# Kernel tuning notes

Measured on AMD Instinct MI355X. Metric: run time of the kernel, lower is better.

Reference implementation:

```python
import jax, jax.numpy as jnp
import numpy as np

N = 100000   # nodes
E = 1600000  # edges
F = 13       # input features
H = 128      # hidden dim
G = 512      # graphs in batch
C = 10       # classes
EPS = 1e-5   # BatchNorm eps


def setup_inputs() -> dict:
    key = jax.random.key(0)
    ks = jax.random.split(key, 12)
    inp = {
        "x": jax.random.normal(ks[0], (N, F), dtype=jnp.float32),
        "edge_index": jax.random.randint(ks[1], (2, E), 0, N, dtype=jnp.int64),
        "batch": jnp.sort(jax.random.randint(ks[2], (N,), 0, G, dtype=jnp.int64)),
        "W1": jax.random.normal(ks[3], (F, H), dtype=jnp.float32) / np.sqrt(F),
        "b1": jnp.zeros((H,), jnp.float32),
        "g1": jnp.ones((H,), jnp.float32), "be1": jnp.zeros((H,), jnp.float32),
        "m1": jnp.zeros((H,), jnp.float32), "v1": jnp.ones((H,), jnp.float32),
        "W2": jax.random.normal(ks[4], (H, H), dtype=jnp.float32) / np.sqrt(H),
        "b2": jnp.zeros((H,), jnp.float32),
        "g2": jnp.ones((H,), jnp.float32), "be2": jnp.zeros((H,), jnp.float32),
        "m2": jnp.zeros((H,), jnp.float32), "v2": jnp.ones((H,), jnp.float32),
        "W3": jax.random.normal(ks[5], (H, H), dtype=jnp.float32) / np.sqrt(H),
        "b3": jnp.zeros((H,), jnp.float32),
        "g3": jnp.ones((H,), jnp.float32), "be3": jnp.zeros((H,), jnp.float32),
        "m3": jnp.zeros((H,), jnp.float32), "v3": jnp.ones((H,), jnp.float32),
        "Wc1": jax.random.normal(ks[6], (H, H // 2), dtype=jnp.float32) / np.sqrt(H),
        "bc1": jnp.zeros((H // 2,), jnp.float32),
        "Wc2": jax.random.normal(ks[7], (H // 2, C), dtype=jnp.float32) / np.sqrt(H // 2),
        "bc2": jnp.zeros((C,), jnp.float32),
    }
    return inp


def reference(x, edge_index, batch,
              W1, b1, g1, be1, m1, v1,
              W2, b2, g2, be2, m2, v2,
              W3, b3, g3, be3, m3, v3,
              Wc1, bc1, Wc2, bc2):
    src, dst = edge_index[0], edge_index[1]
    n = x.shape[0]
    # GCN symmetric norm with self-loops: deg = in-degree(A) + 1
    deg = jax.ops.segment_sum(jnp.ones(src.shape[0], x.dtype), dst, num_segments=n) + 1.0
    dis = jax.lax.rsqrt(deg)                    # D^{-1/2}
    enorm = dis[src] * dis[dst]                 # per-edge norm [E]
    snorm = dis * dis                           # self-loop norm [N]

    def gcn(h, W, b):
        h = h @ W                               # [N,H]
        msg = h[src] * enorm[:, None]           # gather + scale [E,H]
        agg = jax.ops.segment_sum(msg, dst, num_segments=n)  # scatter-add
        return agg + h * snorm[:, None] + b

    def bn(h, g, be, m, v):                     # eval-mode BatchNorm1d
        return (h - m) * jax.lax.rsqrt(v + EPS) * g + be

    h = jax.nn.relu(bn(gcn(x, W1, b1), g1, be1, m1, v1))
    h = jax.nn.relu(bn(gcn(h, W2, b2), g2, be2, m2, v2))
    h = jax.nn.relu(bn(gcn(h, W3, b3), g3, be3, m3, v3))
    # dropout is identity in eval mode

    # global mean pool over graphs
    sums = jax.ops.segment_sum(h, batch, num_segments=G)            # [G,H]
    cnts = jax.ops.segment_sum(jnp.ones(n, h.dtype), batch, num_segments=G)
    pooled = sums / jnp.maximum(cnts, 1.0)[:, None]

    hid = jax.nn.relu(pooled @ Wc1 + bc1)
    logits = hid @ Wc2 + bc2                                        # [G,C]
    return logits
```

## Files before the change

kernel.cpp:

```cpp
#include <hip/hip_runtime.h>
#include <hip/hip_bf16.h>

#define EPS 1e-5f

typedef unsigned short u16;
typedef unsigned int u32;
typedef __attribute__((ext_vector_type(8))) short bf16x8;
typedef __attribute__((ext_vector_type(4))) float f32x4;

__device__ __forceinline__ u32 f2bf(float f) {
  u32 u = __float_as_uint(f);
  return (u + 0x7FFFu + ((u >> 16) & 1u)) >> 16;
}
__device__ __forceinline__ u32 pack2bf(float lo, float hi) {
  return f2bf(lo) | (f2bf(hi) << 16);
}

__device__ __forceinline__ void dacc(float2& a, u32 u) {
  a.x += __uint_as_float(u << 16);
  a.y += __uint_as_float(u & 0xFFFF0000u);
}

__global__ void k_hist_rank(const int* __restrict__ dst, int* __restrict__ cnt,
                            int* __restrict__ rank, int E) {
  int i = blockIdx.x * blockDim.x + threadIdx.x;
  int i8 = i << 3;
  if (i8 + 7 < E) {
    int4 da = *(const int4*)(dst + i8);
    int4 db = *(const int4*)(dst + i8 + 4);
    int r0 = atomicAdd(&cnt[da.x], 1);
    int r1 = atomicAdd(&cnt[da.y], 1);
    int r2 = atomicAdd(&cnt[da.z], 1);
    int r3 = atomicAdd(&cnt[da.w], 1);
    int r4 = atomicAdd(&cnt[db.x], 1);
    int r5 = atomicAdd(&cnt[db.y], 1);
    int r6 = atomicAdd(&cnt[db.z], 1);
    int r7 = atomicAdd(&cnt[db.w], 1);
    *(int4*)(rank + i8)     = make_int4(r0, r1, r2, r3);
    *(int4*)(rank + i8 + 4) = make_int4(r4, r5, r6, r7);
  } else {
    for (int e = i8; e < E; ++e) rank[e] = atomicAdd(&cnt[dst[e]], 1);
  }
}

__global__ void k_prep_nodes(const int* __restrict__ cnt, const float* __restrict__ x,
                             float* __restrict__ dis, int* __restrict__ pdeg,
                             float* __restrict__ xs, int N) {
  int n = blockIdx.x * blockDim.x + threadIdx.x;
  if (n > N) return;
  if (n == N) {
#pragma unroll
    for (int f = 0; f < 16; f += 4)
      *(float4*)(xs + (size_t)N * 16 + f) = make_float4(0.f, 0.f, 0.f, 0.f);
    return;
  }
  int d = cnt[n];
  float dn = rsqrtf((float)d + 1.0f);
  dis[n] = dn;
  pdeg[n] = (d + 3) & ~3;
  float v[16];
#pragma unroll
  for (int f = 0; f < 13; ++f) v[f] = x[(size_t)n * 13 + f] * dn;
  v[13] = v[14] = v[15] = 0.f;
#pragma unroll
  for (int f = 0; f < 16; f += 4)
    *(float4*)(xs + (size_t)n * 16 + f) = make_float4(v[f], v[f+1], v[f+2], v[f+3]);
}

__global__ void k_scan_block(const int* __restrict__ in, int* __restrict__ out,
                             int* __restrict__ bsum, int N) {
  __shared__ int tmp[256];
  int lid = threadIdx.x;
  int i = blockIdx.x * 256 + lid;
  int v = (i < N) ? in[i] : 0;
  tmp[lid] = v;
  __syncthreads();
  for (int off = 1; off < 256; off <<= 1) {
    int t = (lid >= off) ? tmp[lid - off] : 0;
    __syncthreads();
    tmp[lid] += t;
    __syncthreads();
  }
  if (i < N) out[i] = tmp[lid] - v;
  if (lid == 255) bsum[blockIdx.x] = tmp[255];
}

__global__ void k_scan_bsum(const int* __restrict__ bsum, int* __restrict__ bexc, int nb) {
  __shared__ int tmp[512];
  int lid = threadIdx.x;
  int v = (lid < nb) ? bsum[lid] : 0;
  tmp[lid] = v;
  __syncthreads();
  for (int off = 1; off < 512; off <<= 1) {
    int t = (lid >= off) ? tmp[lid - off] : 0;
    __syncthreads();
    tmp[lid] += t;
    __syncthreads();
  }
  if (lid < nb) bexc[lid] = tmp[lid] - v;
}

__global__ void k_add_back_pad(int* __restrict__ offs, const int* __restrict__ bexc,
                               const int* __restrict__ bsum, const int* __restrict__ deg,
                               const int* __restrict__ pdeg, int* __restrict__ csr,
                               int N, int nb) {
  int i = blockIdx.x * 256 + threadIdx.x;
  if (i < N) {
    int o = offs[i] + bexc[blockIdx.x];
    offs[i] = o;
    int b = o + deg[i], e = o + pdeg[i];
    for (int j = b; j < e; ++j) csr[j] = N;
  }
  if (i == 0) offs[N] = bexc[nb - 1] + bsum[nb - 1];
}

__global__ void k_fill_rank(const int* __restrict__ src, const int* __restrict__ dst,
                            const int* __restrict__ rank, const int* __restrict__ offs,
                            int* __restrict__ csr, int E) {
  int i = blockIdx.x * blockDim.x + threadIdx.x;
  int i4 = i << 2;
  if (i4 + 3 < E) {
    int s0 = src[i4], s1 = src[i4 + 1], s2 = src[i4 + 2], s3 = src[i4 + 3];
    int d0 = dst[i4], d1 = dst[i4 + 1], d2 = dst[i4 + 2], d3 = dst[i4 + 3];
    int r0 = rank[i4], r1 = rank[i4 + 1], r2 = rank[i4 + 2], r3 = rank[i4 + 3];
    csr[offs[d0] + r0] = s0;
    csr[offs[d1] + r1] = s1;
    csr[offs[d2] + r2] = s2;
    csr[offs[d3] + r3] = s3;
  } else {
    for (int e = i4; e < E; ++e) csr[offs[dst[e]] + rank[e]] = src[e];
  }
}

__global__ void k_prep_w(const float* __restrict__ W2, const float* __restrict__ W3,
                         const float* __restrict__ b2, const float* __restrict__ g2,
                         const float* __restrict__ be2, const float* __restrict__ m2,
                         const float* __restrict__ v2,
                         const float* __restrict__ b3, const float* __restrict__ g3,
                         const float* __restrict__ be3, const float* __restrict__ m3,
                         const float* __restrict__ v3,
                         u16* __restrict__ Wht2, u16* __restrict__ Wlt2,
                         u16* __restrict__ Wht3, u16* __restrict__ Wlt3,
                         float* __restrict__ sc2, float* __restrict__ tc2,
                         float* __restrict__ sc3, float* __restrict__ tc3) {
  int idx = blockIdx.x * 256 + threadIdx.x;
  int layer = idx >> 14;
  int e = idx & 16383;
  int c = e >> 7, k = e & 127;
  const float* W = layer ? W3 : W2;
  float w = W[k * 128 + c];
  u32 h = f2bf(w);
  float l = w - __uint_as_float(h << 16);
  u16* Wh = layer ? Wht3 : Wht2;
  u16* Wl = layer ? Wlt3 : Wlt2;
  Wh[e] = (u16)h;
  Wl[e] = (u16)f2bf(l);
  if (e < 128) {
    int ch = e;
    const float* gg = layer ? g3 : g2;  const float* vv = layer ? v3 : v2;
    const float* be = layer ? be3 : be2; const float* mm = layer ? m3 : m2;
    const float* bb = layer ? b3 : b2;
    float s = gg[ch] * rsqrtf(vv[ch] + EPS);
    (layer ? sc3 : sc2)[ch] = s;
    (layer ? tc3 : tc2)[ch] = be[ch] + (bb[ch] - mm[ch]) * s;
  }
}

__global__ __launch_bounds__(64) void k_agg16(
    const float* __restrict__ xs, const int* __restrict__ csr,
    const int* __restrict__ offs, const float* __restrict__ dis,
    float* __restrict__ out, int N) {
  int node = (blockIdx.x << 2) + (threadIdx.x >> 4);
  if (node >= N) return;
  int f = threadIdx.x & 15;
  float a0 = xs[(size_t)node * 16 + f];
  float a1 = 0.f, a2 = 0.f, a3 = 0.f;
  int beg = offs[node], end = offs[node + 1];
  for (int i = beg; i < end; i += 4) {
    int4 s4 = *(const int4*)(csr + i);
    a0 += xs[(size_t)s4.x * 16 + f];
    a1 += xs[(size_t)s4.y * 16 + f];
    a2 += xs[(size_t)s4.z * 16 + f];
    a3 += xs[(size_t)s4.w * 16 + f];
  }
  out[(size_t)node * 16 + f] = dis[node] * ((a0 + a1) + (a2 + a3));
}

__global__ __launch_bounds__(256) void k_gemm1(
    const float* __restrict__ ax, const float* __restrict__ W1,
    const float* __restrict__ bb, const float* __restrict__ gg,
    const float* __restrict__ be, const float* __restrict__ mm,
    const float* __restrict__ vv, const float* __restrict__ dis,
    u32* __restrict__ outb, int N) {
  const int lane = threadIdx.x & 63;
  const int wid = blockIdx.x * (blockDim.x >> 6) + (threadIdx.x >> 6);
  const int nw = gridDim.x * (blockDim.x >> 6);
  const int c0 = lane * 2, c1 = c0 + 1;
  float s0 = gg[c0] * rsqrtf(vv[c0] + EPS);
  float t0 = be[c0] + (bb[c0] - mm[c0]) * s0;
  float s1 = gg[c1] * rsqrtf(vv[c1] + EPS);
  float t1 = be[c1] + (bb[c1] - mm[c1]) * s1;
  float w0[13], w1[13];
#pragma unroll
  for (int k = 0; k < 13; ++k) {
    w0[k] = W1[k * 128 + c0];
    w1[k] = W1[k * 128 + c1];
  }
  for (int node = wid; node <= N; node += nw) {
    if (node == N) { outb[(size_t)node * 64 + lane] = 0u; continue; }
    float4 A0 = *(const float4*)(ax + (size_t)node * 16);
    float4 A1 = *(const float4*)(ax + (size_t)node * 16 + 4);
    float4 A2 = *(const float4*)(ax + (size_t)node * 16 + 8);
    float  a12 = ax[(size_t)node * 16 + 12];
    float av[13] = {A0.x, A0.y, A0.z, A0.w, A1.x, A1.y, A1.z, A1.w,
                    A2.x, A2.y, A2.z, A2.w, a12};
    float acc0 = 0.f, acc1 = 0.f;
#pragma unroll
    for (int k = 0; k < 13; ++k) {
      acc0 = fmaf(av[k], w0[k], acc0);
      acc1 = fmaf(av[k], w1[k], acc1);
    }
    float dn = dis[node];
    float o0 = dn * fmaxf(fmaf(acc0, s0, t0), 0.f);
    float o1 = dn * fmaxf(fmaf(acc1, s1, t1), 0.f);
    outb[(size_t)node * 64 + lane] = pack2bf(o0, o1);
  }
}

__global__ __launch_bounds__(256) void k_agg128(
    const u16* __restrict__ hb, const int* __restrict__ csr,
    const int* __restrict__ offs, const float* __restrict__ dis,
    uint4* __restrict__ Ahp, uint4* __restrict__ Alp, int N) {
  int node = (blockIdx.x << 2) + (threadIdx.x >> 6);
  if (node >= N) return;
  node = __builtin_amdgcn_readfirstlane(node);
  const int lane = threadIdx.x & 63;
  const int qt = lane >> 4;
  const int q = lane & 15;
  const uint4* __restrict__ H = (const uint4*)hb;
  int beg = offs[node], end = offs[node + 1];

  float2 z2 = make_float2(0.f, 0.f);
  float2 aA0 = z2, aA1 = z2, aA2 = z2, aA3 = z2;
  float2 aB0 = z2, aB1 = z2, aB2 = z2, aB3 = z2;

  {
    uint4 su = H[(size_t)node * 16 + q];
    if (qt == 0) { dacc(aA0, su.x); dacc(aA1, su.y); dacc(aA2, su.z); dacc(aA3, su.w); }
  }

  int i = beg;
  for (; i + 8 <= end; i += 8) {
    int4 sA = *(const int4*)(csr + i);
    int4 sB = *(const int4*)(csr + i + 4);
    int ea = (qt == 0) ? sA.x : (qt == 1) ? sA.y : (qt == 2) ? sA.z : sA.w;
    int eb = (qt == 0) ? sB.x : (qt == 1) ? sB.y : (qt == 2) ? sB.z : sB.w;
    uint4 uA = H[(size_t)ea * 16 + q];
    uint4 uB = H[(size_t)eb * 16 + q];
    dacc(aA0, uA.x); dacc(aA1, uA.y); dacc(aA2, uA.z); dacc(aA3, uA.w);
    dacc(aB0, uB.x); dacc(aB1, uB.y); dacc(aB2, uB.z); dacc(aB3, uB.w);
  }
  if (i < end) {
    int4 sA = *(const int4*)(csr + i);
    int ea = (qt == 0) ? sA.x : (qt == 1) ? sA.y : (qt == 2) ? sA.z : sA.w;
    uint4 uA = H[(size_t)ea * 16 + q];
    dacc(aA0, uA.x); dacc(aA1, uA.y); dacc(aA2, uA.z); dacc(aA3, uA.w);
  }

  float r[8];
  r[0] = aA0.x + aB0.x; r[1] = aA0.y + aB0.y;
  r[2] = aA1.x + aB1.x; r[3] = aA1.y + aB1.y;
  r[4] = aA2.x + aB2.x; r[5] = aA2.y + aB2.y;
  r[6] = aA3.x + aB3.x; r[7] = aA3.y + aB3.y;
#pragma unroll
  for (int j = 0; j < 8; ++j) {
    r[j] += __shfl_xor(r[j], 16, 64);
    r[j] += __shfl_xor(r[j], 32, 64);
  }
  if (qt == 0) {
    float dn = dis[node];
    uint4 ph, pl;
    u32 hw[8];
#pragma unroll
    for (int j = 0; j < 8; ++j) { r[j] *= dn; hw[j] = f2bf(r[j]); }
    ph.x = hw[0] | (hw[1] << 16);
    ph.y = hw[2] | (hw[3] << 16);
    ph.z = hw[4] | (hw[5] << 16);
    ph.w = hw[6] | (hw[7] << 16);
    float l[8];
#pragma unroll
    for (int j = 0; j < 8; ++j) l[j] = r[j] - __uint_as_float(hw[j] << 16);
    pl.x = pack2bf(l[0], l[1]);
    pl.y = pack2bf(l[2], l[3]);
    pl.z = pack2bf(l[4], l[5]);
    pl.w = pack2bf(l[6], l[7]);
    Ahp[(size_t)node * 16 + q] = ph;
    Alp[(size_t)node * 16 + q] = pl;
  }
}

template <int MODE>
__global__ __launch_bounds__(256) void k_gemm_mfma(
    const u16* __restrict__ Ah, const u16* __restrict__ Al,
    const u16* __restrict__ Wht, const u16* __restrict__ Wlt,
    const float* __restrict__ sc, const float* __restrict__ tc,
    const float* __restrict__ dis,
    u16* __restrict__ outb, int N) {
  const int lane = threadIdx.x & 63;
  const int wv = threadIdx.x >> 6;
  const int r0 = blockIdx.x * 128 + wv * 32;
  const int lr = lane & 15;
  const int kg = lane >> 4;

  bf16x8 ahf[2][4], alf[2][4];
#pragma unroll
  for (int rt = 0; rt < 2; ++rt) {
    int row = min(r0 + rt * 16 + lr, N - 1);
    const bf16x8* pAh = (const bf16x8*)(Ah + (size_t)row * 128 + kg * 8);
    const bf16x8* pAl = (const bf16x8*)(Al + (size_t)row * 128 + kg * 8);
#pragma unroll
    for (int ks = 0; ks < 4; ++ks) {
      ahf[rt][ks] = pAh[ks * 4];
      alf[rt][ks] = pAl[ks * 4];
    }
  }
  float dr[2][4];
  if (MODE == 0) {
#pragma unroll
    for (int rt = 0; rt < 2; ++rt)
#pragma unroll
      for (int j = 0; j < 4; ++j)
        dr[rt][j] = dis[min(r0 + rt * 16 + kg * 4 + j, N - 1)];
  }

#pragma unroll
  for (int ct = 0; ct < 8; ++ct) {
    int c = ct * 16 + lr;
    const bf16x8* pBh = (const bf16x8*)(Wht + (size_t)c * 128 + kg * 8);
    const bf16x8* pBl = (const bf16x8*)(Wlt + (size_t)c * 128 + kg * 8);
    bf16x8 bh[4], bl[4];
#pragma unroll
    for (int ks = 0; ks < 4; ++ks) { bh[ks] = pBh[ks * 4]; bl[ks] = pBl[ks * 4]; }
    float s = sc[c], t = tc[c];
#pragma unroll
    for (int rt = 0; rt < 2; ++rt) {
      f32x4 acc = {0.f, 0.f, 0.f, 0.f};
#pragma unroll
      for (int ks = 0; ks < 4; ++ks) {
        acc = __builtin_amdgcn_mfma_f32_16x16x32_bf16(ahf[rt][ks], bh[ks], acc, 0, 0, 0);
        acc = __builtin_amdgcn_mfma_f32_16x16x32_bf16(alf[rt][ks], bh[ks], acc, 0, 0, 0);
        acc = __builtin_amdgcn_mfma_f32_16x16x32_bf16(ahf[rt][ks], bl[ks], acc, 0, 0, 0);
      }
#pragma unroll
      for (int j = 0; j < 4; ++j) {
        int row = r0 + rt * 16 + kg * 4 + j;
        if (row < N) {
          float o = fmaxf(fmaf(acc[j], s, t), 0.f);
          if (MODE == 0) o *= dr[rt][j];
          outb[(size_t)row * 128 + c] = (u16)f2bf(o);
        }
      }
    }
  }
}

__global__ __launch_bounds__(128) void k_pool(
    const u16* __restrict__ hb, const int* __restrict__ batch,
    float* __restrict__ pooled, int N) {
  int f = threadIdx.x;
  int n0 = blockIdx.x * 128;
  int nEnd = min(n0 + 128, N);
  float acc = 0.f;
  int cur = -1;
  for (int nn = n0; nn < nEnd; ++nn) {
    int g = batch[nn];
    if (g != cur) {
      if (cur >= 0) atomicAdd(&pooled[cur * 128 + f], acc);
      cur = g;
      acc = 0.f;
    }
    acc += __uint_as_float((u32)hb[(size_t)nn * 128 + f] << 16);
  }
  if (cur >= 0) atomicAdd(&pooled[cur * 128 + f], acc);
}

__global__ __launch_bounds__(64) void k_cls(
    const float* __restrict__ pooled, const int* __restrict__ batch, int N,
    const float* __restrict__ Wc1, const float* __restrict__ bc1,
    const float* __restrict__ Wc2, const float* __restrict__ bc2,
    float* __restrict__ out, int G) {
  __shared__ float pm[128];
  __shared__ float hid[64];
  __shared__ float invc_s;
  int g = blockIdx.x, t = threadIdx.x;
  if (t == 0) {
    int lo = 0, hi = N;
    while (lo < hi) { int m = (lo + hi) >> 1; if (batch[m] < g) lo = m + 1; else hi = m; }
    int lb = lo;
    lo = 0; hi = N;
    while (lo < hi) { int m = (lo + hi) >> 1; if (batch[m] <= g) lo = m + 1; else hi = m; }
    invc_s = 1.f / fmaxf((float)(lo - lb), 1.f);
  }
  __syncthreads();
  float invc = invc_s;
  pm[t]      = pooled[g * 128 + t] * invc;
  pm[t + 64] = pooled[g * 128 + 64 + t] * invc;
  __syncthreads();
  float a = bc1[t];
#pragma unroll 8
  for (int k = 0; k < 128; ++k) a = fmaf(pm[k], Wc1[k * 64 + t], a);
  hid[t] = fmaxf(a, 0.f);
  __syncthreads();
  if (t < 10) {
    float a2 = bc2[t];
#pragma unroll
    for (int j = 0; j < 64; ++j) a2 = fmaf(hid[j], Wc2[j * 10 + t], a2);
    out[g * 10 + t] = a2;
  }
}

extern "C" void kernel_launch(void* const* d_in, const int* in_sizes, int n_in,
                              void* d_out, int out_size, void* d_ws, size_t ws_size,
                              hipStream_t stream) {
  const float* x   = (const float*)d_in[0];
  const int*   ei  = (const int*)d_in[1];
  const int* batch = (const int*)d_in[2];
  const float* W1 = (const float*)d_in[3];
  const float* b1 = (const float*)d_in[4];
  const float* g1 = (const float*)d_in[5];
  const float* be1 = (const float*)d_in[6];
  const float* m1 = (const float*)d_in[7];
  const float* v1 = (const float*)d_in[8];
  const float* W2 = (const float*)d_in[9];
  const float* b2 = (const float*)d_in[10];
  const float* g2 = (const float*)d_in[11];
  const float* be2 = (const float*)d_in[12];
  const float* m2 = (const float*)d_in[13];
  const float* v2 = (const float*)d_in[14];
  const float* W3 = (const float*)d_in[15];
  const float* b3 = (const float*)d_in[16];
  const float* g3 = (const float*)d_in[17];
  const float* be3 = (const float*)d_in[18];
  const float* m3 = (const float*)d_in[19];
  const float* v3 = (const float*)d_in[20];
  const float* Wc1 = (const float*)d_in[21];
  const float* bc1 = (const float*)d_in[22];
  const float* Wc2 = (const float*)d_in[23];
  const float* bc2 = (const float*)d_in[24];

  const int N = in_sizes[0] / 13;
  const int E = in_sizes[1] / 2;
  const int G = out_size / 10;
  const int* src = ei;
  const int* dst = ei + E;

  char* ws = (char*)d_ws;
  size_t off = 0;
  auto alloc = [&](size_t bytes) {
    char* p = ws + off;
    off = (off + bytes + 255) & ~(size_t)255;
    return p;
  };
  int*   deg    = (int*)  alloc((size_t)N * 4);
  float* dis    = (float*)alloc((size_t)N * 4);
  int*   pdeg   = (int*)  alloc((size_t)N * 4);
  int*   offs   = (int*)  alloc((size_t)(N + 1) * 4);
  const int nb  = (N + 255) / 256;
  int*   bsum   = (int*)  alloc((size_t)nb * 4);
  int*   bexc   = (int*)  alloc((size_t)nb * 4);
  int*   rank   = (int*)  alloc((size_t)E * 4);
  int*   csr    = (int*)  alloc(((size_t)E + 3 * (size_t)N + 8) * 4);
  u16*   hbf    = (u16*)  alloc((size_t)(N + 1) * 128 * 2);
  u16*   Ahp    = (u16*)  alloc((size_t)N * 128 * 2);
  u16*   Alp    = (u16*)  alloc((size_t)N * 128 * 2);
  float* xs     = (float*)alloc((size_t)(N + 1) * 16 * 4);
  u16*   Wht2   = (u16*)  alloc(16384 * 2);
  u16*   Wlt2   = (u16*)  alloc(16384 * 2);
  u16*   Wht3   = (u16*)  alloc(16384 * 2);
  u16*   Wlt3   = (u16*)  alloc(16384 * 2);
  float* sc2    = (float*)alloc(128 * 4);
  float* tc2    = (float*)alloc(128 * 4);
  float* sc3    = (float*)alloc(128 * 4);
  float* tc3    = (float*)alloc(128 * 4);
  float* pooled = (float*)alloc((size_t)G * 128 * 4);
  float* ax = (float*)Ahp;

  hipMemsetAsync(deg, 0, (size_t)N * 4, stream);
  hipMemsetAsync(pooled, 0, (size_t)G * 128 * 4, stream);

  k_prep_w<<<128, 256, 0, stream>>>(W2, W3, b2, g2, be2, m2, v2, b3, g3, be3, m3, v3,
                                    Wht2, Wlt2, Wht3, Wlt3, sc2, tc2, sc3, tc3);

  const int nE8 = (E + 7) / 8;
  k_hist_rank<<<(nE8 + 255) / 256, 256, 0, stream>>>(dst, deg, rank, E);
  k_prep_nodes<<<(N + 256) / 256, 256, 0, stream>>>(deg, x, dis, pdeg, xs, N);
  k_scan_block<<<nb, 256, 0, stream>>>(pdeg, offs, bsum, N);
  k_scan_bsum<<<1, 512, 0, stream>>>(bsum, bexc, nb);
  k_add_back_pad<<<nb, 256, 0, stream>>>(offs, bexc, bsum, deg, pdeg, csr, N, nb);
  const int nE4 = (E + 3) / 4;
  k_fill_rank<<<(nE4 + 255) / 256, 256, 0, stream>>>(src, dst, rank, offs, csr, E);

  k_agg16<<<(N + 3) / 4, 64, 0, stream>>>(xs, csr, offs, dis, ax, N);
  k_gemm1<<<1024, 256, 0, stream>>>(ax, W1, b1, g1, be1, m1, v1, dis, (u32*)hbf, N);

  const int gemmGrid = (N + 127) / 128;
  k_agg128<<<(N + 3) / 4, 256, 0, stream>>>(hbf, csr, offs, dis,
                                            (uint4*)Ahp, (uint4*)Alp, N);
  k_gemm_mfma<0><<<gemmGrid, 256, 0, stream>>>(Ahp, Alp, Wht2, Wlt2, sc2, tc2, dis,
                                               hbf, N);
  k_agg128<<<(N + 3) / 4, 256, 0, stream>>>(hbf, csr, offs, dis,
                                            (uint4*)Ahp, (uint4*)Alp, N);
  k_gemm_mfma<1><<<gemmGrid, 256, 0, stream>>>(Ahp, Alp, Wht3, Wlt3, sc3, tc3, dis,
                                               hbf, N);

  k_pool<<<(N + 127) / 128, 128, 0, stream>>>(hbf, batch, pooled, N);
  k_cls<<<G, 64, 0, stream>>>(pooled, batch, N, Wc1, bc1, Wc2, bc2, (float*)d_out, G);
}
```

Measured before the change: 532.6 us.

## Fuse neighbor aggregation with MFMA GEMM via LDS staging for layers two and three

Merges the per-node 128-wide gather-aggregate kernel and the split-bf16 MFMA GEMM into one kernel. Each block aggregates 64 nodes into swizzled shared memory, then runs the GEMM straight from LDS, so the hi/lo aggregate arrays no longer round-trip through global memory. This needs ping-pong output buffers (hbf/hbf2). The two memsets are folded into the weight-prep kernel, which also zeroes the padding row. Each wave now handles 16 nodes in sequence, which cuts latency-hiding parallelism in the gather phase and leaves the MFMA phase waiting on the slowest wave in the block.

```diff
diff --git a/kernel.cpp b/kernel.cpp
--- a/kernel.cpp
+++ b/kernel.cpp
@@ -142,7 +142,9 @@
                          u16* __restrict__ Wht2, u16* __restrict__ Wlt2,
                          u16* __restrict__ Wht3, u16* __restrict__ Wlt3,
                          float* __restrict__ sc2, float* __restrict__ tc2,
-                         float* __restrict__ sc3, float* __restrict__ tc3) {
+                         float* __restrict__ sc3, float* __restrict__ tc3,
+                         int* __restrict__ deg, float* __restrict__ pooled,
+                         u32* __restrict__ hbf2_padrow, int N, int GP) {
   int idx = blockIdx.x * 256 + threadIdx.x;
   int layer = idx >> 14;
   int e = idx & 16383;
@@ -164,6 +166,9 @@
     (layer ? sc3 : sc2)[ch] = s;
     (layer ? tc3 : tc2)[ch] = be[ch] + (bb[ch] - mm[ch]) * s;
   }
+  for (int i = idx; i < N; i += 32768) deg[i] = 0;
+  for (int i = idx; i < GP; i += 32768) pooled[i] = 0.f;
+  if (idx < 64) hbf2_padrow[idx] = 0u;
 }
 
 __global__ __launch_bounds__(64) void k_agg16(
@@ -227,112 +232,103 @@
   }
 }
 
-__global__ __launch_bounds__(256) void k_agg128(
+template <int MODE>
+__global__ __launch_bounds__(256) void k_agg_gemm(
     const u16* __restrict__ hb, const int* __restrict__ csr,
     const int* __restrict__ offs, const float* __restrict__ dis,
-    uint4* __restrict__ Ahp, uint4* __restrict__ Alp, int N) {
-  int node = (blockIdx.x << 2) + (threadIdx.x >> 6);
-  if (node >= N) return;
-  node = __builtin_amdgcn_readfirstlane(node);
+    const u16* __restrict__ Wht, const u16* __restrict__ Wlt,
+    const float* __restrict__ sc, const float* __restrict__ tc,
+    u16* __restrict__ outb, int N) {
+  __shared__ uint4 Ash[64][16];
+  __shared__ uint4 Asl[64][16];
+  const int wv = threadIdx.x >> 6;
   const int lane = threadIdx.x & 63;
   const int qt = lane >> 4;
   const int q = lane & 15;
+  const int base = blockIdx.x * 64;
   const uint4* __restrict__ H = (const uint4*)hb;
-  int beg = offs[node], end = offs[node + 1];
-
-  float2 z2 = make_float2(0.f, 0.f);
-  float2 aA0 = z2, aA1 = z2, aA2 = z2, aA3 = z2;
-  float2 aB0 = z2, aB1 = z2, aB2 = z2, aB3 = z2;
-
-  {
-    uint4 su = H[(size_t)node * 16 + q];
-    if (qt == 0) { dacc(aA0, su.x); dacc(aA1, su.y); dacc(aA2, su.z); dacc(aA3, su.w); }
-  }
-
-  int i = beg;
-  for (; i + 8 <= end; i += 8) {
-    int4 sA = *(const int4*)(csr + i);
-    int4 sB = *(const int4*)(csr + i + 4);
-    int ea = (qt == 0) ? sA.x : (qt == 1) ? sA.y : (qt == 2) ? sA.z : sA.w;
-    int eb = (qt == 0) ? sB.x : (qt == 1) ? sB.y : (qt == 2) ? sB.z : sB.w;
-    uint4 uA = H[(size_t)ea * 16 + q];
-    uint4 uB = H[(size_t)eb * 16 + q];
-    dacc(aA0, uA.x); dacc(aA1, uA.y); dacc(aA2, uA.z); dacc(aA3, uA.w);
-    dacc(aB0, uB.x); dacc(aB1, uB.y); dacc(aB2, uB.z); dacc(aB3, uB.w);
-  }
-  if (i < end) {
-    int4 sA = *(const int4*)(csr + i);
-    int ea = (qt == 0) ? sA.x : (qt == 1) ? sA.y : (qt == 2) ? sA.z : sA.w;
-    uint4 uA = H[(size_t)ea * 16 + q];
-    dacc(aA0, uA.x); dacc(aA1, uA.y); dacc(aA2, uA.z); dacc(aA3, uA.w);
-  }
-
-  float r[8];
-  r[0] = aA0.x + aB0.x; r[1] = aA0.y + aB0.y;
-  r[2] = aA1.x + aB1.x; r[3] = aA1.y + aB1.y;
-  r[4] = aA2.x + aB2.x; r[5] = aA2.y + aB2.y;
-  r[6] = aA3.x + aB3.x; r[7] = aA3.y + aB3.y;
-#pragma unroll
-  for (int j = 0; j < 8; ++j) {
-    r[j] += __shfl_xor(r[j], 16, 64);
-    r[j] += __shfl_xor(r[j], 32, 64);
-  }
-  if (qt == 0) {
-    float dn = dis[node];
-    uint4 ph, pl;
-    u32 hw[8];
-#pragma unroll
-    for (int j = 0; j < 8; ++j) { r[j] *= dn; hw[j] = f2bf(r[j]); }
-    ph.x = hw[0] | (hw[1] << 16);
-    ph.y = hw[2] | (hw[3] << 16);
-    ph.z = hw[4] | (hw[5] << 16);
-    ph.w = hw[6] | (hw[7] << 16);
-    float l[8];
-#pragma unroll
-    for (int j = 0; j < 8; ++j) l[j] = r[j] - __uint_as_float(hw[j] << 16);
-    pl.x = pack2bf(l[0], l[1]);
-    pl.y = pack2bf(l[2], l[3]);
-    pl.z = pack2bf(l[4], l[5]);
-    pl.w = pack2bf(l[6], l[7]);
-    Ahp[(size_t)node * 16 + q] = ph;
-    Alp[(size_t)node * 16 + q] = pl;
-  }
-}
-
-template <int MODE>
-__global__ __launch_bounds__(256) void k_gemm_mfma(
-    const u16* __restrict__ Ah, const u16* __restrict__ Al,
-    const u16* __restrict__ Wht, const u16* __restrict__ Wlt,
-    const float* __restrict__ sc, const float* __restrict__ tc,
-    const float* __restrict__ dis,
-    u16* __restrict__ outb, int N) {
-  const int lane = threadIdx.x & 63;
-  const int wv = threadIdx.x >> 6;
-  const int r0 = blockIdx.x * 128 + wv * 32;
+
+  for (int t = 0; t < 16; ++t) {
+    int row = wv * 16 + t;
+    int node = base + row;
+    if (node >= N) break;
+    int beg = offs[node], end = offs[node + 1];
+
+    float2 z2 = make_float2(0.f, 0.f);
+    float2 aA0 = z2, aA1 = z2, aA2 = z2, aA3 = z2;
+    float2 aB0 = z2, aB1 = z2, aB2 = z2, aB3 = z2;
+    {
+      uint4 su = H[(size_t)node * 16 + q];
+      if (qt == 0) { dacc(aA0, su.x); dacc(aA1, su.y); dacc(aA2, su.z); dacc(aA3, su.w); }
+    }
+    int i = beg;
+    for (; i + 8 <= end; i += 8) {
+      int4 sA = *(const int4*)(csr + i);
+      int4 sB = *(const int4*)(csr + i + 4);
+      int ea = (qt == 0) ? sA.x : (qt == 1) ? sA.y : (qt == 2) ? sA.z : sA.w;
+      int eb = (qt == 0) ? sB.x : (qt == 1) ? sB.y : (qt == 2) ? sB.z : sB.w;
+      uint4 uA = H[(size_t)ea * 16 + q];
+      uint4 uB = H[(size_t)eb * 16 + q];
+      dacc(aA0, uA.x); dacc(aA1, uA.y); dacc(aA2, uA.z); dacc(aA3, uA.w);
+      dacc(aB0, uB.x); dacc(aB1, uB.y); dacc(aB2, uB.z); dacc(aB3, uB.w);
+    }
+    if (i < end) {
+      int4 sA = *(const int4*)(csr + i);
+      int ea = (qt == 0) ? sA.x : (qt == 1) ? sA.y : (qt == 2) ? sA.z : sA.w;
+      uint4 uA = H[(size_t)ea * 16 + q];
+      dacc(aA0, uA.x); dacc(aA1, uA.y); dacc(aA2, uA.z); dacc(aA3, uA.w);
+    }
+    float r[8];
+    r[0] = aA0.x + aB0.x; r[1] = aA0.y + aB0.y;
+    r[2] = aA1.x + aB1.x; r[3] = aA1.y + aB1.y;
+    r[4] = aA2.x + aB2.x; r[5] = aA2.y + aB2.y;
+    r[6] = aA3.x + aB3.x; r[7] = aA3.y + aB3.y;
+#pragma unroll
+    for (int j = 0; j < 8; ++j) {
+      r[j] += __shfl_xor(r[j], 16, 64);
+      r[j] += __shfl_xor(r[j], 32, 64);
+    }
+    if (qt == 0) {
+      float dn = dis[node];
+      u32 hw[8];
+      uint4 ph, pl;
+#pragma unroll
+      for (int j = 0; j < 8; ++j) { r[j] *= dn; hw[j] = f2bf(r[j]); }
+      ph.x = hw[0] | (hw[1] << 16);
+      ph.y = hw[2] | (hw[3] << 16);
+      ph.z = hw[4] | (hw[5] << 16);
+      ph.w = hw[6] | (hw[7] << 16);
+      float l[8];
+#pragma unroll
+      for (int j = 0; j < 8; ++j) l[j] = r[j] - __uint_as_float(hw[j] << 16);
+      pl.x = pack2bf(l[0], l[1]);
+      pl.y = pack2bf(l[2], l[3]);
+      pl.z = pack2bf(l[4], l[5]);
+      pl.w = pack2bf(l[6], l[7]);
+      int sw = q ^ (row & 15);
+      Ash[row][sw] = ph;
+      Asl[row][sw] = pl;
+    }
+  }
+  __syncthreads();
+
   const int lr = lane & 15;
   const int kg = lane >> 4;
-
-  bf16x8 ahf[2][4], alf[2][4];
-#pragma unroll
-  for (int rt = 0; rt < 2; ++rt) {
-    int row = min(r0 + rt * 16 + lr, N - 1);
-    const bf16x8* pAh = (const bf16x8*)(Ah + (size_t)row * 128 + kg * 8);
-    const bf16x8* pAl = (const bf16x8*)(Al + (size_t)row * 128 + kg * 8);
-#pragma unroll
-    for (int ks = 0; ks < 4; ++ks) {
-      ahf[rt][ks] = pAh[ks * 4];
-      alf[rt][ks] = pAl[ks * 4];
-    }
-  }
-  float dr[2][4];
+  const int rowbase = wv * 16;
+  const int arow = rowbase + lr;
+  bf16x8 ah[4], al[4];
+#pragma unroll
+  for (int ks = 0; ks < 4; ++ks) {
+    int b = (kg + 4 * ks) ^ (arow & 15);
+    ah[ks] = *(const bf16x8*)&Ash[arow][b];
+    al[ks] = *(const bf16x8*)&Asl[arow][b];
+  }
+  float dr[4];
   if (MODE == 0) {
 #pragma unroll
-    for (int rt = 0; rt < 2; ++rt)
-#pragma unroll
-      for (int j = 0; j < 4; ++j)
-        dr[rt][j] = dis[min(r0 + rt * 16 + kg * 4 + j, N - 1)];
-  }
-
+    for (int j = 0; j < 4; ++j)
+      dr[j] = dis[min(base + rowbase + kg * 4 + j, N - 1)];
+  }
 #pragma unroll
   for (int ct = 0; ct < 8; ++ct) {
     int c = ct * 16 + lr;
@@ -342,23 +338,20 @@
 #pragma unroll
     for (int ks = 0; ks < 4; ++ks) { bh[ks] = pBh[ks * 4]; bl[ks] = pBl[ks * 4]; }
     float s = sc[c], t = tc[c];
-#pragma unroll
-    for (int rt = 0; rt < 2; ++rt) {
-      f32x4 acc = {0.f, 0.f, 0.f, 0.f};
-#pragma unroll
-      for (int ks = 0; ks < 4; ++ks) {
-        acc = __builtin_amdgcn_mfma_f32_16x16x32_bf16(ahf[rt][ks], bh[ks], acc, 0, 0, 0);
-        acc = __builtin_amdgcn_mfma_f32_16x16x32_bf16(alf[rt][ks], bh[ks], acc, 0, 0, 0);
-        acc = __builtin_amdgcn_mfma_f32_16x16x32_bf16(ahf[rt][ks], bl[ks], acc, 0, 0, 0);
-      }
-#pragma unroll
-      for (int j = 0; j < 4; ++j) {
-        int row = r0 + rt * 16 + kg * 4 + j;
-        if (row < N) {
-          float o = fmaxf(fmaf(acc[j], s, t), 0.f);
-          if (MODE == 0) o *= dr[rt][j];
-          outb[(size_t)row * 128 + c] = (u16)f2bf(o);
-        }
+    f32x4 acc = {0.f, 0.f, 0.f, 0.f};
+#pragma unroll
+    for (int ks = 0; ks < 4; ++ks) {
+      acc = __builtin_amdgcn_mfma_f32_16x16x32_bf16(ah[ks], bh[ks], acc, 0, 0, 0);
+      acc = __builtin_amdgcn_mfma_f32_16x16x32_bf16(al[ks], bh[ks], acc, 0, 0, 0);
+      acc = __builtin_amdgcn_mfma_f32_16x16x32_bf16(ah[ks], bl[ks], acc, 0, 0, 0);
+    }
+#pragma unroll
+    for (int j = 0; j < 4; ++j) {
+      int row = base + rowbase + kg * 4 + j;
+      if (row < N) {
+        float o = fmaxf(fmaf(acc[j], s, t), 0.f);
+        if (MODE == 0) o *= dr[j];
+        outb[(size_t)row * 128 + c] = (u16)f2bf(o);
       }
     }
   }
@@ -471,9 +464,9 @@
   int*   rank   = (int*)  alloc((size_t)E * 4);
   int*   csr    = (int*)  alloc(((size_t)E + 3 * (size_t)N + 8) * 4);
   u16*   hbf    = (u16*)  alloc((size_t)(N + 1) * 128 * 2);
-  u16*   Ahp    = (u16*)  alloc((size_t)N * 128 * 2);
-  u16*   Alp    = (u16*)  alloc((size_t)N * 128 * 2);
+  u16*   hbf2   = (u16*)  alloc((size_t)(N + 1) * 128 * 2);
   float* xs     = (float*)alloc((size_t)(N + 1) * 16 * 4);
+  float* ax     = (float*)alloc((size_t)N * 16 * 4);
   u16*   Wht2   = (u16*)  alloc(16384 * 2);
   u16*   Wlt2   = (u16*)  alloc(16384 * 2);
   u16*   Wht3   = (u16*)  alloc(16384 * 2);
@@ -483,13 +476,11 @@
   float* sc3    = (float*)alloc(128 * 4);
   float* tc3    = (float*)alloc(128 * 4);
   float* pooled = (float*)alloc((size_t)G * 128 * 4);
-  float* ax = (float*)Ahp;
-
-  hipMemsetAsync(deg, 0, (size_t)N * 4, stream);
-  hipMemsetAsync(pooled, 0, (size_t)G * 128 * 4, stream);
 
   k_prep_w<<<128, 256, 0, stream>>>(W2, W3, b2, g2, be2, m2, v2, b3, g3, be3, m3, v3,
-                                    Wht2, Wlt2, Wht3, Wlt3, sc2, tc2, sc3, tc3);
+                                    Wht2, Wlt2, Wht3, Wlt3, sc2, tc2, sc3, tc3,
+                                    deg, pooled, (u32*)(hbf2 + (size_t)N * 128),
+                                    N, G * 128);
 
   const int nE8 = (E + 7) / 8;
   k_hist_rank<<<(nE8 + 255) / 256, 256, 0, stream>>>(dst, deg, rank, E);
@@ -503,15 +494,11 @@
   k_agg16<<<(N + 3) / 4, 64, 0, stream>>>(xs, csr, offs, dis, ax, N);
   k_gemm1<<<1024, 256, 0, stream>>>(ax, W1, b1, g1, be1, m1, v1, dis, (u32*)hbf, N);
 
-  const int gemmGrid = (N + 127) / 128;
-  k_agg128<<<(N + 3) / 4, 256, 0, stream>>>(hbf, csr, offs, dis,
-                                            (uint4*)Ahp, (uint4*)Alp, N);
-  k_gemm_mfma<0><<<gemmGrid, 256, 0, stream>>>(Ahp, Alp, Wht2, Wlt2, sc2, tc2, dis,
-                                               hbf, N);
-  k_agg128<<<(N + 3) / 4, 256, 0, stream>>>(hbf, csr, offs, dis,
-                                            (uint4*)Ahp, (uint4*)Alp, N);
-  k_gemm_mfma<1><<<gemmGrid, 256, 0, stream>>>(Ahp, Alp, Wht3, Wlt3, sc3, tc3, dis,
-                                               hbf, N);
+  const int fusedGrid = (N + 63) / 64;
+  k_agg_gemm<0><<<fusedGrid, 256, 0, stream>>>(hbf, csr, offs, dis,
+                                               Wht2, Wlt2, sc2, tc2, hbf2, N);
+  k_agg_gemm<1><<<fusedGrid, 256, 0, stream>>>(hbf2, csr, offs, dis,
+                                               Wht3, Wlt3, sc3, tc3, hbf, N);
 
   k_pool<<<(N + 127) / 128, 128, 0, stream>>>(hbf, batch, pooled, N);
   k_cls<<<G, 64, 0, stream>>>(pooled, batch, N, Wc1, bc1, Wc2, bc2, (float*)d_out, G);
```

Measured after the change: 642.3 us. +20.6%, slower.
